# Optimization experiments

Hardware: AMD Instinct MI355X
Metric: run time of the kernel (lower is better)

The kernel has to match this reference:

```python
import jax, jax.numpy as jnp
import numpy as np

V, E, D, B, C = 100000, 256, 128, 8192, 10  # vocab, embedding_size, context_size, batch, window


def setup_inputs() -> dict:
    key = jax.random.key(0)
    ks = jax.random.split(key, 11)
    s = 0.02
    return {
        "x": jax.random.randint(ks[0], (B,), 0, V),
        "context": jax.random.randint(ks[1], (B, C), 0, V),
        "W_emb": jax.random.normal(ks[2], (V, E), jnp.float32) * s,
        "M_w": jax.random.normal(ks[3], (D, E), jnp.float32) * s,
        "M_b": jnp.zeros((D,), jnp.float32),
        "U_w": jax.random.normal(ks[4], (D, 2 * D), jnp.float32) * s,
        "U_b": jnp.zeros((D,), jnp.float32),
        "W_w": jax.random.normal(ks[5], (D, 2 * D), jnp.float32) * s,
        "W_b": jnp.zeros((D,), jnp.float32),
        "prior_mus": jax.random.normal(ks[6], (V, D), jnp.float32) * s,
        # covariance diagonal must be positive for a valid Gaussian (torch would
        # Cholesky-fail otherwise); sample in [0.1, 1.0)
        "prior_sigmas": jax.random.uniform(ks[7], (V, D), jnp.float32, 0.1, 1.0),
    }


def reference(x, context, W_emb, M_w, M_b, U_w, U_b, W_w, W_b, prior_mus, prior_sigmas):
    emb_x = W_emb[x]                       # [B, E]
    emb_c = W_emb[context]                 # [B, C, E]
    Rw = emb_x @ M_w.T + M_b               # [B, D]  (repeated over C slots below)
    Rc = jnp.einsum('bce,de->bcd', emb_c, M_w) + M_b  # [B, C, D]
    RwC = jnp.broadcast_to(Rw[:, None, :], Rc.shape)   # repeat(len(context), 1)
    h = jax.nn.relu(jnp.concatenate([RwC, Rc], axis=-1)).sum(axis=1)  # [B, 2D]
    mu = h @ U_w.T + U_b                   # posterior mean  [B, D]
    sigma = jax.nn.softplus(h @ W_w.T + W_b)  # posterior cov diag [B, D]
    m0 = prior_mus[x]                      # prior mean      [B, D]
    s0 = prior_sigmas[x]                   # prior cov diag  [B, D]
    # closed-form KL(N(m0, diag(s0)) || N(mu, diag(sigma)))
    d = jnp.float32(D)
    kl = 0.5 * ((s0 / sigma).sum(-1)
                + ((mu - m0) ** 2 / sigma).sum(-1)
                - d
                + jnp.log(sigma).sum(-1) - jnp.log(s0).sum(-1))
    return kl  # [B]
```

## Files before the change

### kernel.cpp

```cpp
#include <hip/hip_runtime.h>
#include <hip/hip_bf16.h>
#include <math.h>


#define CTXN  10
#define DDIM  128
#define WS_M   0
#define WS_UW  32768
#define WS_H   98304

typedef short bf16x8 __attribute__((ext_vector_type(8)));
typedef float f32x4  __attribute__((ext_vector_type(4)));

__device__ __forceinline__ uint2 cvt4(float4 v) {
    union { __hip_bfloat162 h2; unsigned u; } a, b;
    a.h2 = __float22bfloat162_rn(make_float2(v.x, v.y));
    b.h2 = __float22bfloat162_rn(make_float2(v.z, v.w));
    return make_uint2(a.u, b.u);
}

__device__ __forceinline__ float softplusf(float v) {
    return fmaxf(v, 0.0f) + log1pf(expf(-fabsf(v)));
}

__global__ __launch_bounds__(256) void k_cvt(
    const float* __restrict__ M_w, const float* __restrict__ U_w,
    const float* __restrict__ W_w, unsigned short* __restrict__ ws)
{
    int which = blockIdx.x >> 5;
    int i = ((blockIdx.x & 31) << 8) | threadIdx.x;
    const float* src = (which == 0) ? M_w : (which == 1) ? U_w : W_w;
    float4 v = ((const float4*)src)[i];
    *(uint2*)&ws[which * 32768 + i * 4] = cvt4(v);
}

#define BT1   8
#define ROWSP 96
#define LP2   264

__global__ __launch_bounds__(512, 6) void bsg_h(
    const int* __restrict__ x, const int* __restrict__ ctx,
    const float* __restrict__ W_emb, const float* __restrict__ M_b,
    const unsigned short* __restrict__ wsr, unsigned short* __restrict__ hws)
{
    __shared__ __align__(16) unsigned short A_s[ROWSP * LP2];
    __shared__ int idx_s[ROWSP];

    const int tid  = threadIdx.x;
    const int b0   = blockIdx.x * BT1;
    const int w    = tid >> 6;
    const int lane = tid & 63;
    const int l15  = lane & 15;
    const int lg   = lane >> 4;

    if (tid < ROWSP) {
        int c = tid >> 3, b = b0 + (tid & 7);
        idx_s[tid] = (c >= 11) ? 0 : ((c == 0) ? x[b] : ctx[b * CTXN + (c - 1)]);
    }
    __syncthreads();

    const int rs = tid >> 6;
    const int qs = tid & 63;
    const float4* We = (const float4*)W_emb;

    {
        float4 rr[6];
#pragma unroll
        for (int s = 0; s < 6; ++s)
            rr[s] = We[(size_t)idx_s[rs + 8 * s] * 64 + qs];
#pragma unroll
        for (int s = 0; s < 6; ++s)
            *(uint2*)&A_s[(rs + 8 * s) * LP2 + 4 * qs] = cvt4(rr[s]);
#pragma unroll
        for (int s = 6; s < 12; ++s)
            rr[s - 6] = We[(size_t)idx_s[rs + 8 * s] * 64 + qs];
#pragma unroll
        for (int s = 6; s < 12; ++s)
            *(uint2*)&A_s[(rs + 8 * s) * LP2 + 4 * qs] = cvt4(rr[s - 6]);
    }
    __syncthreads();

    const unsigned short* Mb_bf = wsr + WS_M;
    const int mrow = 16 * w + l15;
    f32x4 acc[6] = {};
#pragma unroll
    for (int ch = 0; ch < 4; ++ch) {
        bf16x8 m0 = *(const bf16x8*)&Mb_bf[mrow * 256 + 64 * ch + 8 * lg];
        bf16x8 m1 = *(const bf16x8*)&Mb_bf[mrow * 256 + 64 * ch + 32 + 8 * lg];
#pragma unroll
        for (int mt = 0; mt < 6; ++mt) {
            bf16x8 a0 = *(const bf16x8*)&A_s[(16 * mt + l15) * LP2 + 64 * ch + 8 * lg];
            bf16x8 a1 = *(const bf16x8*)&A_s[(16 * mt + l15) * LP2 + 64 * ch + 32 + 8 * lg];
            acc[mt] = __builtin_amdgcn_mfma_f32_16x16x32_bf16(a0, m0, acc[mt], 0, 0, 0);
            acc[mt] = __builtin_amdgcn_mfma_f32_16x16x32_bf16(a1, m1, acc[mt], 0, 0, 0);
        }
    }

    const int dg = 16 * w + l15;
    const float mb = M_b[dg];
    float p1[4] = {0, 0, 0, 0}, p2[4] = {0, 0, 0, 0};
#pragma unroll
    for (int mt = 0; mt < 6; ++mt) {
#pragma unroll
        for (int q = 0; q < 4; ++q) {
            float r = fmaxf(acc[mt][q] + mb, 0.0f);
            if (lg < 2) { if (mt == 0) p1[q] = r; else p2[q] += r; }
            else        { if (mt < 5)  p2[q] += r; }
        }
    }
#pragma unroll
    for (int q = 0; q < 4; ++q) {
        float other = __shfl_xor(p2[q], 32);
        if (lg < 2) {
            int b = 4 * lg + q;
            __hip_bfloat16 t1 = __float2bfloat16(10.0f * p1[q]);
            __hip_bfloat16 t2 = __float2bfloat16(p2[q] + other);
            hws[(size_t)(b0 + b) * 256 + dg]       = *(unsigned short*)&t1;
            hws[(size_t)(b0 + b) * 256 + 128 + dg] = *(unsigned short*)&t2;
        }
    }
}

#define BT2  32
#define HLP  264

__global__ __launch_bounds__(512, 4) void bsg_kl(
    const int* __restrict__ x, const float* __restrict__ U_b,
    const float* __restrict__ W_b, const float* __restrict__ pmu,
    const float* __restrict__ psg, const unsigned short* __restrict__ wsr,
    float* __restrict__ out)
{
    __shared__ __align__(16) unsigned short H_s[BT2 * HLP];
    __shared__ float P_s[BT2 * 8];

    const int tid  = threadIdx.x;
    const int b0   = blockIdx.x * BT2;
    const int w    = tid >> 6;
    const int lane = tid & 63;
    const int l15  = lane & 15;
    const int lg   = lane >> 4;
    const int d    = 16 * w + l15;

    float pm[2][4], ps[2][4];
#pragma unroll
    for (int mt = 0; mt < 2; ++mt)
#pragma unroll
        for (int q = 0; q < 4; ++q) {
            int xb = x[b0 + 16 * mt + 4 * lg + q];
            pm[mt][q] = pmu[(size_t)xb * DDIM + d];
            ps[mt][q] = psg[(size_t)xb * DDIM + d];
        }

    const unsigned short* hws = wsr + WS_H;
#pragma unroll
    for (int s = 0; s < 2; ++s) {
        int it = tid + 512 * s;
        int r = it >> 5, q = it & 31;
        *(uint4*)&H_s[r * HLP + 8 * q] =
            *(const uint4*)&hws[(size_t)(b0 + r) * 256 + 8 * q];
    }
    __syncthreads();

    const unsigned short* UWb = wsr + WS_UW;
    f32x4 acc2[2][2] = {};
#pragma unroll
    for (int ks = 0; ks < 8; ++ks) {
        bf16x8 bu = *(const bf16x8*)&UWb[d * 256 + 32 * ks + 8 * lg];
        bf16x8 bw = *(const bf16x8*)&UWb[(128 + d) * 256 + 32 * ks + 8 * lg];
#pragma unroll
        for (int mt = 0; mt < 2; ++mt) {
            bf16x8 hf = *(const bf16x8*)&H_s[(16 * mt + l15) * HLP + 32 * ks + 8 * lg];
            acc2[mt][0] = __builtin_amdgcn_mfma_f32_16x16x32_bf16(hf, bu, acc2[mt][0], 0, 0, 0);
            acc2[mt][1] = __builtin_amdgcn_mfma_f32_16x16x32_bf16(hf, bw, acc2[mt][1], 0, 0, 0);
        }
    }

    const float ub = U_b[d], wb = W_b[d];
#pragma unroll
    for (int mt = 0; mt < 2; ++mt) {
#pragma unroll
        for (int q = 0; q < 4; ++q) {
            int rb = 16 * mt + 4 * lg + q;
            float mu = acc2[mt][0][q] + ub;
            float sg = softplusf(acc2[mt][1][q] + wb);
            float dm = mu - pm[mt][q];
            float p  = ps[mt][q] / sg + dm * dm / sg + logf(sg) - logf(ps[mt][q]);
            p += __shfl_xor(p, 1);
            p += __shfl_xor(p, 2);
            p += __shfl_xor(p, 4);
            p += __shfl_xor(p, 8);
            if (l15 == 0) P_s[rb * 8 + w] = p;
        }
    }
    __syncthreads();
    if (tid < BT2) {
        float s = 0.0f;
#pragma unroll
        for (int k = 0; k < 8; ++k) s += P_s[tid * 8 + k];
        out[b0 + tid] = 0.5f * (s - (float)DDIM);
    }
}

extern "C" void kernel_launch(void* const* d_in, const int* in_sizes, int n_in,
                              void* d_out, int out_size, void* d_ws, size_t ws_size,
                              hipStream_t stream) {
    const int*   x     = (const int*)  d_in[0];
    const int*   ctx   = (const int*)  d_in[1];
    const float* W_emb = (const float*)d_in[2];
    const float* M_w   = (const float*)d_in[3];
    const float* M_b   = (const float*)d_in[4];
    const float* U_w   = (const float*)d_in[5];
    const float* U_b   = (const float*)d_in[6];
    const float* W_w   = (const float*)d_in[7];
    const float* W_b   = (const float*)d_in[8];
    const float* pmu   = (const float*)d_in[9];
    const float* psg   = (const float*)d_in[10];
    float* out = (float*)d_out;
    unsigned short* ws = (unsigned short*)d_ws;

    k_cvt<<<dim3(96), dim3(256), 0, stream>>>(M_w, U_w, W_w, ws);
    bsg_h<<<dim3(8192 / BT1), dim3(512), 0, stream>>>(x, ctx, W_emb, M_b,
                                                      ws, ws + WS_H);
    bsg_kl<<<dim3(8192 / BT2), dim3(512), 0, stream>>>(x, U_b, W_b, pmu, psg,
                                                       ws, out);
}
```

Before: 41.62 us.

## Fuse weight conversion into embedding kernel and drop separate convert launch

Removes the standalone bf16 conversion kernel. Each bsg_h wave now loads its M_w rows in fp32 and converts them into registers directly, and the first 32 blocks also convert U_w/W_w into the workspace for the later KL kernel. This saves one kernel launch and the serialized dependency on it. In exchange every block rereads fp32 M_w, register pressure rises (launch bounds lowered to 4 waves per SIMD), and a few blocks do extra conversion work.

Result: slower. 45.21 us (+8.6%).

```diff
diff --git a/kernel.cpp b/kernel.cpp
--- a/kernel.cpp
+++ b/kernel.cpp
@@ -5,9 +5,8 @@
 
 #define CTXN  10
 #define DDIM  128
-#define WS_M   0
-#define WS_UW  32768
-#define WS_H   98304
+#define WS_UW  0
+#define WS_H   65536
 
 typedef short bf16x8 __attribute__((ext_vector_type(8)));
 typedef float f32x4  __attribute__((ext_vector_type(4)));
@@ -19,29 +18,29 @@
     return make_uint2(a.u, b.u);
 }
 
+__device__ __forceinline__ bf16x8 cvt8(float4 a, float4 b) {
+    union { __hip_bfloat162 h2[4]; bf16x8 v; } u;
+    u.h2[0] = __float22bfloat162_rn(make_float2(a.x, a.y));
+    u.h2[1] = __float22bfloat162_rn(make_float2(a.z, a.w));
+    u.h2[2] = __float22bfloat162_rn(make_float2(b.x, b.y));
+    u.h2[3] = __float22bfloat162_rn(make_float2(b.z, b.w));
+    return u.v;
+}
+
 __device__ __forceinline__ float softplusf(float v) {
     return fmaxf(v, 0.0f) + log1pf(expf(-fabsf(v)));
-}
-
-__global__ __launch_bounds__(256) void k_cvt(
-    const float* __restrict__ M_w, const float* __restrict__ U_w,
-    const float* __restrict__ W_w, unsigned short* __restrict__ ws)
-{
-    int which = blockIdx.x >> 5;
-    int i = ((blockIdx.x & 31) << 8) | threadIdx.x;
-    const float* src = (which == 0) ? M_w : (which == 1) ? U_w : W_w;
-    float4 v = ((const float4*)src)[i];
-    *(uint2*)&ws[which * 32768 + i * 4] = cvt4(v);
 }
 
 #define BT1   8
 #define ROWSP 96
 #define LP2   264
 
-__global__ __launch_bounds__(512, 6) void bsg_h(
+__global__ __launch_bounds__(512, 4) void bsg_h(
     const int* __restrict__ x, const int* __restrict__ ctx,
-    const float* __restrict__ W_emb, const float* __restrict__ M_b,
-    const unsigned short* __restrict__ wsr, unsigned short* __restrict__ hws)
+    const float* __restrict__ W_emb, const float* __restrict__ M_w,
+    const float* __restrict__ M_b,   const float* __restrict__ U_w,
+    const float* __restrict__ W_w,
+    unsigned short* __restrict__ ws, unsigned short* __restrict__ hws)
 {
     __shared__ __align__(16) unsigned short A_s[ROWSP * LP2];
     __shared__ int idx_s[ROWSP];
@@ -53,6 +52,24 @@
     const int l15  = lane & 15;
     const int lg   = lane >> 4;
 
+    const int mrow = 16 * w + l15;
+    const float4* Mw4 = (const float4*)M_w;
+    bf16x8 mreg[8];
+#pragma unroll
+    for (int kk = 0; kk < 8; ++kk) {
+        float4 a = Mw4[mrow * 64 + 8 * kk + 2 * lg];
+        float4 b = Mw4[mrow * 64 + 8 * kk + 2 * lg + 1];
+        mreg[kk] = cvt8(a, b);
+    }
+
+    if (blockIdx.x < 32) {
+        int it = blockIdx.x * 512 + tid;
+        int n = it >> 6, q = it & 63;
+        const float* src = (n < DDIM) ? U_w : W_w;
+        float4 v = ((const float4*)src)[(n & 127) * 64 + q];
+        *(uint2*)&ws[WS_UW + n * 256 + 4 * q] = cvt4(v);
+    }
+
     if (tid < ROWSP) {
         int c = tid >> 3, b = b0 + (tid & 7);
         idx_s[tid] = (c >= 11) ? 0 : ((c == 0) ? x[b] : ctx[b * CTXN + (c - 1)]);
@@ -62,7 +79,6 @@
     const int rs = tid >> 6;
     const int qs = tid & 63;
     const float4* We = (const float4*)W_emb;
-
     {
         float4 rr[6];
 #pragma unroll
@@ -80,19 +96,15 @@
     }
     __syncthreads();
 
-    const unsigned short* Mb_bf = wsr + WS_M;
-    const int mrow = 16 * w + l15;
     f32x4 acc[6] = {};
 #pragma unroll
     for (int ch = 0; ch < 4; ++ch) {
-        bf16x8 m0 = *(const bf16x8*)&Mb_bf[mrow * 256 + 64 * ch + 8 * lg];
-        bf16x8 m1 = *(const bf16x8*)&Mb_bf[mrow * 256 + 64 * ch + 32 + 8 * lg];
 #pragma unroll
         for (int mt = 0; mt < 6; ++mt) {
             bf16x8 a0 = *(const bf16x8*)&A_s[(16 * mt + l15) * LP2 + 64 * ch + 8 * lg];
             bf16x8 a1 = *(const bf16x8*)&A_s[(16 * mt + l15) * LP2 + 64 * ch + 32 + 8 * lg];
-            acc[mt] = __builtin_amdgcn_mfma_f32_16x16x32_bf16(a0, m0, acc[mt], 0, 0, 0);
-            acc[mt] = __builtin_amdgcn_mfma_f32_16x16x32_bf16(a1, m1, acc[mt], 0, 0, 0);
+            acc[mt] = __builtin_amdgcn_mfma_f32_16x16x32_bf16(a0, mreg[2 * ch],     acc[mt], 0, 0, 0);
+            acc[mt] = __builtin_amdgcn_mfma_f32_16x16x32_bf16(a1, mreg[2 * ch + 1], acc[mt], 0, 0, 0);
         }
     }
 
@@ -218,9 +230,8 @@
     float* out = (float*)d_out;
     unsigned short* ws = (unsigned short*)d_ws;
 
-    k_cvt<<<dim3(96), dim3(256), 0, stream>>>(M_w, U_w, W_w, ws);
-    bsg_h<<<dim3(8192 / BT1), dim3(512), 0, stream>>>(x, ctx, W_emb, M_b,
-                                                      ws, ws + WS_H);
+    bsg_h<<<dim3(8192 / BT1), dim3(512), 0, stream>>>(x, ctx, W_emb, M_w, M_b,
+                                                      U_w, W_w, ws, ws + WS_H);
     bsg_kl<<<dim3(8192 / BT2), dim3(512), 0, stream>>>(x, U_b, W_b, pmu, psg,
                                                        ws, out);
 }
```
